# Kernel optimization log

Hardware: AMD Instinct MI355X
Metric: run time of the kernel (lower is better)

## Reference

```python
import jax, jax.numpy as jnp
import numpy as np

ALPHA = 0.2  # LeakyReLU negative slope


def setup_inputs() -> dict:
    key = jax.random.key(0)
    k1, k2, k3, k4 = jax.random.split(key, 4)
    B, N, Fin, Fout = 8, 2048, 256, 256
    h = jax.random.normal(k1, (B, N, Fin), dtype=jnp.float32)
    # random 0/1 adjacency with guaranteed self-loops so every row has a neighbor
    adj = jax.random.randint(k2, (N, N), 0, 2).astype(jnp.float32)
    adj = jnp.maximum(adj, jnp.eye(N, dtype=jnp.float32))
    # xavier_uniform with gain=1.414
    def xavier(k, shape, gain=1.414):
        fan_in, fan_out = shape[0], shape[1]
        a = gain * np.sqrt(6.0 / (fan_in + fan_out))
        return jax.random.uniform(k, shape, dtype=jnp.float32, minval=-a, maxval=a)
    W = xavier(k3, (Fin, Fout))
    a = xavier(k4, (2 * Fout, 1))
    return {"h": h, "adj_matrix": adj, "W": W, "a": a}


def reference(h, adj_matrix, W, a):
    # h: [B, N, Fin], adj_matrix: [N, N], W: [Fin, Fout], a: [2*Fout, 1]
    Fout = W.shape[1]
    Wh = jnp.einsum("bnf,fo->bno", h, W)            # [B, N, Fout]
    a1, a2 = a[:Fout, 0], a[Fout:, 0]                 # split additive attention vector
    # e[b,i,j] = leakyrelu(Wh[b,i]@a1 + Wh[b,j]@a2) — equals concat([Wh_i,Wh_j])@a
    s1 = Wh @ a1                                      # [B, N]
    s2 = Wh @ a2                                      # [B, N]
    e = s1[:, :, None] + s2[:, None, :]               # [B, N, N]
    e = jnp.where(e >= 0, e, ALPHA * e)               # LeakyReLU
    e = jnp.where(adj_matrix[None] == 0, -jnp.inf, e)  # mask non-edges
    attention = jax.nn.softmax(e, axis=-1)            # [B, N, N]
    # dropout is identity in eval mode (training=False)
    h_prime = jnp.einsum("bij,bjo->bio", attention, Wh)
    return h_prime
```

## Files before the change

### kernel.cpp

```cpp
#include <hip/hip_runtime.h>
#include <cstdint>

#define NN 2048
#define LOG2E 1.4426950408889634f

typedef __attribute__((ext_vector_type(8))) short bf16x8;
typedef __attribute__((ext_vector_type(4))) float f32x4;

__device__ __forceinline__ unsigned short f2bf(float x){
  union { float f; unsigned u; } v; v.f = x;
  unsigned r = v.u + 0x7FFFu + ((v.u >> 16) & 1u);
  return (unsigned short)(r >> 16);
}
__device__ __forceinline__ unsigned pack2(float a, float b){
  return (unsigned)f2bf(a) | ((unsigned)f2bf(b) << 16);
}
__device__ __forceinline__ unsigned permpack(unsigned hi, unsigned lo){
  return __builtin_amdgcn_perm(hi, lo, 0x07060302u);
}

__global__ __launch_bounds__(256) void k_prep(const float* __restrict__ adj,
                                              const float* __restrict__ W,
                                              unsigned long long* __restrict__ ab,
                                              unsigned short* __restrict__ Wt){
  int tid = threadIdx.x;
  if (blockIdx.x < 2048){
    int i = blockIdx.x;
    int w = tid >> 6, lane = tid & 63;
    #pragma unroll
    for (int seg = 0; seg < 8; seg++){
      int j = seg * 256 + tid;
      unsigned long long m = __ballot(adj[(size_t)i * NN + j] != 0.0f);
      if (lane == 0) ab[i * 32 + seg * 4 + w] = m;
    }
  } else {
    int g = (blockIdx.x - 2048) * 256 + tid;
    int o = g >> 8, k = g & 255;
    Wt[g] = f2bf(W[k * 256 + o]);
  }
}

__global__ __launch_bounds__(512, 2) void k_fused_gemm(const float* __restrict__ h,
                                                       const unsigned short* __restrict__ Wt,
                                                       const float* __restrict__ a,
                                                       unsigned short* __restrict__ WhT,
                                                       float* __restrict__ s1c,
                                                       float* __restrict__ s2c){
  __shared__ __align__(16) unsigned short As[2][64 * 72];
  __shared__ __align__(16) unsigned short Ts[256 * 72];
  __shared__ float s1p[8][64], s2p[8][64];
  const int tid = threadIdx.x;
  const int r0 = blockIdx.x * 64;
  const int b  = r0 >> 11;
  const int i0 = r0 & (NN - 1);
  const int w = tid >> 6, lane = tid & 63, lhi = lane >> 4, llo = lane & 15;
  const int wc = w * 32;

  f32x4 acc[4][2];
  #pragma unroll
  for (int i = 0; i < 4; i++)
    #pragma unroll
    for (int j = 0; j < 2; j++){ acc[i][j][0]=0.f; acc[i][j][1]=0.f; acc[i][j][2]=0.f; acc[i][j][3]=0.f; }

  const int ar = tid >> 3;
  const int as_ = (tid & 7) * 8;

  float4 hv[4][2];
  #pragma unroll
  for (int t = 0; t < 4; t++){
    const float* hp = h + (size_t)(r0 + ar) * 256 + t * 64 + as_;
    hv[t][0] = *(const float4*)hp;
    hv[t][1] = *(const float4*)(hp + 4);
  }

  auto loadB = [&](int k0, bf16x8* dst){
    #pragma unroll
    for (int ot = 0; ot < 2; ot++)
      #pragma unroll
      for (int kk = 0; kk < 2; kk++)
        dst[ot * 2 + kk] = *(const bf16x8*)(Wt + (size_t)(wc + ot * 16 + llo) * 256 + k0 + kk * 32 + lhi * 8);
  };

  bf16x8 bfr[2][4];
  loadB(0, bfr[0]);

  #pragma unroll
  for (int t = 0; t < 4; t++){
    uint4 q = make_uint4(pack2(hv[t][0].x, hv[t][0].y), pack2(hv[t][0].z, hv[t][0].w),
                         pack2(hv[t][1].x, hv[t][1].y), pack2(hv[t][1].z, hv[t][1].w));
    *(uint4*)&As[t & 1][ar * 72 + as_] = q;
    __syncthreads();
    if (t < 3) loadB((t + 1) * 64, bfr[(t + 1) & 1]);
    bf16x8 af[2][4];
    #pragma unroll
    for (int kk = 0; kk < 2; kk++)
      #pragma unroll
      for (int it = 0; it < 4; it++)
        af[kk][it] = *(const bf16x8*)&As[t & 1][(it * 16 + llo) * 72 + kk * 32 + lhi * 8];
    #pragma unroll
    for (int kk = 0; kk < 2; kk++)
      #pragma unroll
      for (int it = 0; it < 4; it++)
        #pragma unroll
        for (int ot = 0; ot < 2; ot++)
          acc[it][ot] = __builtin_amdgcn_mfma_f32_16x16x32_bf16(af[kk][it], bfr[t & 1][ot * 2 + kk], acc[it][ot], 0, 0, 0);
  }

  float a1v[2], a2v[2];
  #pragma unroll
  for (int ot = 0; ot < 2; ot++){
    a1v[ot] = a[wc + ot * 16 + llo] * LOG2E;
    a2v[ot] = a[256 + wc + ot * 16 + llo] * LOG2E;
  }
  #pragma unroll
  for (int it = 0; it < 4; it++){
    #pragma unroll
    for (int q = 0; q < 4; q++){
      float p1 = acc[it][0][q] * a1v[0] + acc[it][1][q] * a1v[1];
      float p2 = acc[it][0][q] * a2v[0] + acc[it][1][q] * a2v[1];
      #pragma unroll
      for (int o = 1; o < 16; o <<= 1){ p1 += __shfl_xor(p1, o); p2 += __shfl_xor(p2, o); }
      if (llo == 0){
        s1p[w][it * 16 + lhi * 4 + q] = p1;
        s2p[w][it * 16 + lhi * 4 + q] = p2;
      }
    }
  }

  #pragma unroll
  for (int it = 0; it < 4; it++){
    #pragma unroll
    for (int ot = 0; ot < 2; ot++){
      int o = wc + ot * 16 + llo;
      uint2 u = make_uint2(pack2(acc[it][ot][0], acc[it][ot][1]),
                           pack2(acc[it][ot][2], acc[it][ot][3]));
      *(uint2*)&Ts[o * 72 + it * 16 + lhi * 4] = u;
    }
  }
  __syncthreads();

  if (tid < 64){
    float t1 = 0.f, t2 = 0.f;
    #pragma unroll
    for (int g = 0; g < 8; g++){ t1 += s1p[g][tid]; t2 += s2p[g][tid]; }
    s1c[r0 + tid] = t1;
    s2c[r0 + tid] = t2;
  }
  #pragma unroll
  for (int p = 0; p < 4; p++){
    int o = p * 64 + (tid >> 3), col = (tid & 7) * 8;
    *(uint4*)(WhT + (size_t)(b * 256 + o) * 2048 + i0 + col) = *(const uint4*)&Ts[o * 72 + col];
  }
}

__global__ __launch_bounds__(512, 2) void k_attn(const float* __restrict__ s1c,
                                                 const float* __restrict__ s2c,
                                                 const unsigned short* __restrict__ WhT,
                                                 const unsigned long long* __restrict__ ab,
                                                 float* __restrict__ out){
  __shared__ __align__(16) float s2s[2048];
  __shared__ __align__(16) unsigned short Ps[2][64 * 72];
  __shared__ __align__(16) unsigned char bitsB[64 * 264];
  __shared__ float s1s[64], lin[64], red[8];
  const int tid = threadIdx.x;
  const int bid = blockIdx.x;
  const int b = bid & 7, i0 = (bid >> 3) * 64;
  const int w = tid >> 6, lane = tid & 63, lhi = lane >> 4, llo = lane & 15;
  const int wc = w * 32;

  float4 v = ((const float4*)(s2c + (size_t)b * NN))[tid];
  ((float4*)s2s)[tid] = v;
  float vmax = fmaxf(fmaxf(v.x, v.y), fmaxf(v.z, v.w));
  #pragma unroll
  for (int o = 32; o; o >>= 1) vmax = fmaxf(vmax, __shfl_xor(vmax, o));
  if (lane == 0) red[w] = vmax;
  if (tid < 64) s1s[tid] = s1c[(size_t)b * NN + i0 + tid];
  #pragma unroll
  for (int k = 0; k < 4; k++){
    int g = k * 512 + tid;
    unsigned long long mw = ab[(size_t)i0 * 32 + g];
    *(unsigned long long*)&bitsB[(g >> 5) * 264 + (g & 31) * 8] = mw;
  }
  __syncthreads();
  float m2 = red[0];
  #pragma unroll
  for (int g = 1; g < 8; g++) m2 = fmaxf(m2, red[g]);

  const int pi = tid >> 3;
  const int e8 = tid & 7;
  const int pj = e8 * 8;
  const float s1v = s1s[pi];
  const float xm = s1v + m2;
  const float mv = fmaxf(xm, 0.2f * xm);
  const float c1 = s1v - mv;
  const float c2 = 0.2f * s1v - mv;
  float rs = 0.f;

  f32x4 acc[4][2];
  #pragma unroll
  for (int i = 0; i < 4; i++)
    #pragma unroll
    for (int j = 0; j < 2; j++){ acc[i][j][0]=0.f; acc[i][j][1]=0.f; acc[i][j][2]=0.f; acc[i][j][3]=0.f; }

  auto loadB = [&](int j0, bf16x8* dst){
    #pragma unroll
    for (int ot = 0; ot < 2; ot++)
      #pragma unroll
      for (int kk = 0; kk < 2; kk++)
        dst[ot * 2 + kk] = *(const bf16x8*)(WhT + (size_t)(b * 256 + wc + ot * 16 + llo) * 2048 + j0 + kk * 32 + lhi * 8);
  };

  unsigned pu[8];
  auto computeP = [&](int tn){
    unsigned bits = bitsB[pi * 264 + tn * 8 + e8];
    const float* sp = &s2s[tn * 64 + pj];
    float4 xa = *(const float4*)sp;
    float4 xb = *(const float4*)(sp + 4);
    float xs[8] = {xa.x, xa.y, xa.z, xa.w, xb.x, xb.y, xb.z, xb.w};
    #pragma unroll
    for (int e = 0; e < 8; e++){
      float s2v = xs[e];
      float y = fmaxf(s2v + c1, __builtin_fmaf(0.2f, s2v, c2));
      float p = __builtin_amdgcn_exp2f(y);
      unsigned m = ((bits >> e) & 1u) ? 0xFFFF0000u : 0u;
      unsigned u = __float_as_uint(p) & m;
      rs += __uint_as_float(u);
      pu[e] = u;
    }
  };

  auto stageBody = [&](int t, int BUF, bf16x8* curB, bf16x8* nxtB, bool last){
    uint4 q = make_uint4(permpack(pu[1], pu[0]), permpack(pu[3], pu[2]),
                         permpack(pu[5], pu[4]), permpack(pu[7], pu[6]));
    *(uint4*)&Ps[BUF][pi * 72 + pj] = q;
    __syncthreads();
    if (!last) loadB((t + 1) * 64, nxtB);
    bf16x8 af[2][4];
    #pragma unroll
    for (int kk = 0; kk < 2; kk++)
      #pragma unroll
      for (int it = 0; it < 4; it++)
        af[kk][it] = *(const bf16x8*)&Ps[BUF][(it * 16 + llo) * 72 + kk * 32 + lhi * 8];
    if (!last) computeP(t + 1);
    #pragma unroll
    for (int kk = 0; kk < 2; kk++)
      #pragma unroll
      for (int it = 0; it < 4; it++)
        #pragma unroll
        for (int ot = 0; ot < 2; ot++)
          acc[it][ot] = __builtin_amdgcn_mfma_f32_16x16x32_bf16(af[kk][it], curB[ot * 2 + kk], acc[it][ot], 0, 0, 0);
  };

  bf16x8 bA[4], bB[4];
  loadB(0, bA);
  computeP(0);
  for (int t2 = 0; t2 < 32; t2 += 2){
    stageBody(t2,     0, bA, bB, false);
    stageBody(t2 + 1, 1, bB, bA, t2 + 1 == 31);
  }

  rs += __shfl_xor(rs, 1);
  rs += __shfl_xor(rs, 2);
  rs += __shfl_xor(rs, 4);
  if (e8 == 0) lin[pi] = 1.0f / rs;
  __syncthreads();

  #pragma unroll
  for (int it = 0; it < 4; it++){
    #pragma unroll
    for (int ot = 0; ot < 2; ot++){
      int col = wc + ot * 16 + llo;
      #pragma unroll
      for (int q = 0; q < 4; q++){
        int row = it * 16 + lhi * 4 + q;
        out[(size_t)(b * NN + i0 + row) * 256 + col] = acc[it][ot][q] * lin[row];
      }
    }
  }
}

extern "C" void kernel_launch(void* const* d_in, const int* in_sizes, int n_in,
                              void* d_out, int out_size, void* d_ws, size_t ws_size,
                              hipStream_t stream) {
  const float* h   = (const float*)d_in[0];
  const float* adj = (const float*)d_in[1];
  const float* W   = (const float*)d_in[2];
  const float* a   = (const float*)d_in[3];
  float* out = (float*)d_out;

  char* ws = (char*)d_ws;
  unsigned short* WhT      = (unsigned short*)(ws);
  unsigned short* Wt       = (unsigned short*)(ws + 8388608);
  unsigned long long* ab   = (unsigned long long*)(ws + 8519680);
  float* s1c               = (float*)(ws + 9043968);
  float* s2c               = (float*)(ws + 9109504);

  hipLaunchKernelGGL(k_prep,       dim3(2304), dim3(256), 0, stream, adj, W, ab, Wt);
  hipLaunchKernelGGL(k_fused_gemm, dim3(256),  dim3(512), 0, stream, h, Wt, a, WhT, s1c, s2c);
  hipLaunchKernelGGL(k_attn,       dim3(256),  dim3(512), 0, stream, s1c, s2c, WhT, ab, out);
}
```

Measured before the change: 136.6 us.

## Shrink row tiles and split attention output columns across more blocks

Both kernels move from 512-thread blocks with 64-row tiles to 256-thread blocks with 32-row tiles. The projection GEMM grid grows to 512 blocks, and the attention kernel grid grows to 1024 blocks by also splitting the 256 output columns into two halves of 128. The aim is more resident waves per CU to hide latency, and to fill the GPU better than one large block per CU. The cost is that each attention row's softmax probabilities (exp and mask work) are now computed twice, once per column half. The WhT tile is fetched per half, and the s2 vector and mask bits are loaded per block. A sync is also added before overwriting the double-buffered A tile in the GEMM.

```diff
diff --git a/kernel.cpp b/kernel.cpp
--- a/kernel.cpp
+++ b/kernel.cpp
@@ -40,27 +40,27 @@
   }
 }
 
-__global__ __launch_bounds__(512, 2) void k_fused_gemm(const float* __restrict__ h,
+__global__ __launch_bounds__(256, 2) void k_fused_gemm(const float* __restrict__ h,
                                                        const unsigned short* __restrict__ Wt,
                                                        const float* __restrict__ a,
                                                        unsigned short* __restrict__ WhT,
                                                        float* __restrict__ s1c,
                                                        float* __restrict__ s2c){
-  __shared__ __align__(16) unsigned short As[2][64 * 72];
-  __shared__ __align__(16) unsigned short Ts[256 * 72];
-  __shared__ float s1p[8][64], s2p[8][64];
+  __shared__ __align__(16) unsigned short As[2][32 * 72];
+  __shared__ __align__(16) unsigned short Ts[256 * 40];
+  __shared__ float s1p[4][32], s2p[4][32];
   const int tid = threadIdx.x;
-  const int r0 = blockIdx.x * 64;
+  const int r0 = blockIdx.x * 32;
   const int b  = r0 >> 11;
   const int i0 = r0 & (NN - 1);
   const int w = tid >> 6, lane = tid & 63, lhi = lane >> 4, llo = lane & 15;
-  const int wc = w * 32;
-
-  f32x4 acc[4][2];
-  #pragma unroll
-  for (int i = 0; i < 4; i++)
-    #pragma unroll
-    for (int j = 0; j < 2; j++){ acc[i][j][0]=0.f; acc[i][j][1]=0.f; acc[i][j][2]=0.f; acc[i][j][3]=0.f; }
+  const int wc = w * 64;
+
+  f32x4 acc[2][4];
+  #pragma unroll
+  for (int i = 0; i < 2; i++)
+    #pragma unroll
+    for (int j = 0; j < 4; j++){ acc[i][j][0]=0.f; acc[i][j][1]=0.f; acc[i][j][2]=0.f; acc[i][j][3]=0.f; }
 
   const int ar = tid >> 3;
   const int as_ = (tid & 7) * 8;
@@ -75,49 +75,54 @@
 
   auto loadB = [&](int k0, bf16x8* dst){
     #pragma unroll
-    for (int ot = 0; ot < 2; ot++)
+    for (int ot = 0; ot < 4; ot++)
       #pragma unroll
       for (int kk = 0; kk < 2; kk++)
         dst[ot * 2 + kk] = *(const bf16x8*)(Wt + (size_t)(wc + ot * 16 + llo) * 256 + k0 + kk * 32 + lhi * 8);
   };
 
-  bf16x8 bfr[2][4];
+  bf16x8 bfr[2][8];
   loadB(0, bfr[0]);
 
   #pragma unroll
   for (int t = 0; t < 4; t++){
     uint4 q = make_uint4(pack2(hv[t][0].x, hv[t][0].y), pack2(hv[t][0].z, hv[t][0].w),
                          pack2(hv[t][1].x, hv[t][1].y), pack2(hv[t][1].z, hv[t][1].w));
+    if (t) __syncthreads();
     *(uint4*)&As[t & 1][ar * 72 + as_] = q;
     __syncthreads();
     if (t < 3) loadB((t + 1) * 64, bfr[(t + 1) & 1]);
-    bf16x8 af[2][4];
+    bf16x8 af[2][2];
     #pragma unroll
     for (int kk = 0; kk < 2; kk++)
       #pragma unroll
-      for (int it = 0; it < 4; it++)
+      for (int it = 0; it < 2; it++)
         af[kk][it] = *(const bf16x8*)&As[t & 1][(it * 16 + llo) * 72 + kk * 32 + lhi * 8];
     #pragma unroll
     for (int kk = 0; kk < 2; kk++)
       #pragma unroll
-      for (int it = 0; it < 4; it++)
+      for (int it = 0; it < 2; it++)
         #pragma unroll
-        for (int ot = 0; ot < 2; ot++)
+        for (int ot = 0; ot < 4; ot++)
           acc[it][ot] = __builtin_amdgcn_mfma_f32_16x16x32_bf16(af[kk][it], bfr[t & 1][ot * 2 + kk], acc[it][ot], 0, 0, 0);
   }
 
-  float a1v[2], a2v[2];
-  #pragma unroll
-  for (int ot = 0; ot < 2; ot++){
+  float a1v[4], a2v[4];
+  #pragma unroll
+  for (int ot = 0; ot < 4; ot++){
     a1v[ot] = a[wc + ot * 16 + llo] * LOG2E;
     a2v[ot] = a[256 + wc + ot * 16 + llo] * LOG2E;
   }
   #pragma unroll
-  for (int it = 0; it < 4; it++){
+  for (int it = 0; it < 2; it++){
     #pragma unroll
     for (int q = 0; q < 4; q++){
-      float p1 = acc[it][0][q] * a1v[0] + acc[it][1][q] * a1v[1];
-      float p2 = acc[it][0][q] * a2v[0] + acc[it][1][q] * a2v[1];
+      float p1 = 0.f, p2 = 0.f;
+      #pragma unroll
+      for (int ot = 0; ot < 4; ot++){
+        p1 += acc[it][ot][q] * a1v[ot];
+        p2 += acc[it][ot][q] * a2v[ot];
+      }
       #pragma unroll
       for (int o = 1; o < 16; o <<= 1){ p1 += __shfl_xor(p1, o); p2 += __shfl_xor(p2, o); }
       if (llo == 0){
@@ -128,63 +133,67 @@
   }
 
   #pragma unroll
-  for (int it = 0; it < 4; it++){
-    #pragma unroll
-    for (int ot = 0; ot < 2; ot++){
+  for (int it = 0; it < 2; it++){
+    #pragma unroll
+    for (int ot = 0; ot < 4; ot++){
       int o = wc + ot * 16 + llo;
       uint2 u = make_uint2(pack2(acc[it][ot][0], acc[it][ot][1]),
                            pack2(acc[it][ot][2], acc[it][ot][3]));
-      *(uint2*)&Ts[o * 72 + it * 16 + lhi * 4] = u;
+      *(uint2*)&Ts[o * 40 + it * 16 + lhi * 4] = u;
     }
   }
   __syncthreads();
 
-  if (tid < 64){
+  if (tid < 32){
     float t1 = 0.f, t2 = 0.f;
     #pragma unroll
-    for (int g = 0; g < 8; g++){ t1 += s1p[g][tid]; t2 += s2p[g][tid]; }
+    for (int g = 0; g < 4; g++){ t1 += s1p[g][tid]; t2 += s2p[g][tid]; }
     s1c[r0 + tid] = t1;
     s2c[r0 + tid] = t2;
   }
   #pragma unroll
   for (int p = 0; p < 4; p++){
-    int o = p * 64 + (tid >> 3), col = (tid & 7) * 8;
-    *(uint4*)(WhT + (size_t)(b * 256 + o) * 2048 + i0 + col) = *(const uint4*)&Ts[o * 72 + col];
-  }
-}
-
-__global__ __launch_bounds__(512, 2) void k_attn(const float* __restrict__ s1c,
+    int o = p * 64 + (tid >> 2), col = (tid & 3) * 8;
+    *(uint4*)(WhT + (size_t)(b * 256 + o) * 2048 + i0 + col) = *(const uint4*)&Ts[o * 40 + col];
+  }
+}
+
+__global__ __launch_bounds__(256, 4) void k_attn(const float* __restrict__ s1c,
                                                  const float* __restrict__ s2c,
                                                  const unsigned short* __restrict__ WhT,
                                                  const unsigned long long* __restrict__ ab,
                                                  float* __restrict__ out){
   __shared__ __align__(16) float s2s[2048];
-  __shared__ __align__(16) unsigned short Ps[2][64 * 72];
-  __shared__ __align__(16) unsigned char bitsB[64 * 264];
-  __shared__ float s1s[64], lin[64], red[8];
+  __shared__ __align__(16) unsigned short Ps[2][32 * 72];
+  __shared__ __align__(16) unsigned char bitsB[32 * 264];
+  __shared__ float s1s[32], lin[32], red[4];
   const int tid = threadIdx.x;
   const int bid = blockIdx.x;
-  const int b = bid & 7, i0 = (bid >> 3) * 64;
+  const int b = bid & 7;
+  const int r = bid >> 3;
+  const int i0 = (r & 63) * 32;
+  const int o0 = (r >> 6) * 128;
   const int w = tid >> 6, lane = tid & 63, lhi = lane >> 4, llo = lane & 15;
-  const int wc = w * 32;
-
-  float4 v = ((const float4*)(s2c + (size_t)b * NN))[tid];
-  ((float4*)s2s)[tid] = v;
-  float vmax = fmaxf(fmaxf(v.x, v.y), fmaxf(v.z, v.w));
+  const int co = o0 + w * 32;
+
+  float4 v0 = ((const float4*)(s2c + (size_t)b * NN))[tid];
+  float4 v1 = ((const float4*)(s2c + (size_t)b * NN))[tid + 256];
+  ((float4*)s2s)[tid]       = v0;
+  ((float4*)s2s)[tid + 256] = v1;
+  float vmax = fmaxf(fmaxf(fmaxf(v0.x, v0.y), fmaxf(v0.z, v0.w)),
+                     fmaxf(fmaxf(v1.x, v1.y), fmaxf(v1.z, v1.w)));
   #pragma unroll
   for (int o = 32; o; o >>= 1) vmax = fmaxf(vmax, __shfl_xor(vmax, o));
   if (lane == 0) red[w] = vmax;
-  if (tid < 64) s1s[tid] = s1c[(size_t)b * NN + i0 + tid];
+  if (tid < 32) s1s[tid] = s1c[(size_t)b * NN + i0 + tid];
   #pragma unroll
   for (int k = 0; k < 4; k++){
-    int g = k * 512 + tid;
+    int g = k * 256 + tid;
     unsigned long long mw = ab[(size_t)i0 * 32 + g];
     *(unsigned long long*)&bitsB[(g >> 5) * 264 + (g & 31) * 8] = mw;
   }
   __syncthreads();
-  float m2 = red[0];
-  #pragma unroll
-  for (int g = 1; g < 8; g++) m2 = fmaxf(m2, red[g]);
+  float m2 = fmaxf(fmaxf(red[0], red[1]), fmaxf(red[2], red[3]));
 
   const int pi = tid >> 3;
   const int e8 = tid & 7;
@@ -196,9 +205,9 @@
   const float c2 = 0.2f * s1v - mv;
   float rs = 0.f;
 
-  f32x4 acc[4][2];
-  #pragma unroll
-  for (int i = 0; i < 4; i++)
+  f32x4 acc[2][2];
+  #pragma unroll
+  for (int i = 0; i < 2; i++)
     #pragma unroll
     for (int j = 0; j < 2; j++){ acc[i][j][0]=0.f; acc[i][j][1]=0.f; acc[i][j][2]=0.f; acc[i][j][3]=0.f; }
 
@@ -207,7 +216,7 @@
     for (int ot = 0; ot < 2; ot++)
       #pragma unroll
       for (int kk = 0; kk < 2; kk++)
-        dst[ot * 2 + kk] = *(const bf16x8*)(WhT + (size_t)(b * 256 + wc + ot * 16 + llo) * 2048 + j0 + kk * 32 + lhi * 8);
+        dst[ot * 2 + kk] = *(const bf16x8*)(WhT + (size_t)(b * 256 + co + ot * 16 + llo) * 2048 + j0 + kk * 32 + lhi * 8);
   };
 
   unsigned pu[8];
@@ -235,17 +244,17 @@
     *(uint4*)&Ps[BUF][pi * 72 + pj] = q;
     __syncthreads();
     if (!last) loadB((t + 1) * 64, nxtB);
-    bf16x8 af[2][4];
+    bf16x8 af[2][2];
     #pragma unroll
     for (int kk = 0; kk < 2; kk++)
       #pragma unroll
-      for (int it = 0; it < 4; it++)
+      for (int it = 0; it < 2; it++)
         af[kk][it] = *(const bf16x8*)&Ps[BUF][(it * 16 + llo) * 72 + kk * 32 + lhi * 8];
     if (!last) computeP(t + 1);
     #pragma unroll
     for (int kk = 0; kk < 2; kk++)
       #pragma unroll
-      for (int it = 0; it < 4; it++)
+      for (int it = 0; it < 2; it++)
         #pragma unroll
         for (int ot = 0; ot < 2; ot++)
           acc[it][ot] = __builtin_amdgcn_mfma_f32_16x16x32_bf16(af[kk][it], curB[ot * 2 + kk], acc[it][ot], 0, 0, 0);
@@ -266,10 +275,10 @@
   __syncthreads();
 
   #pragma unroll
-  for (int it = 0; it < 4; it++){
+  for (int it = 0; it < 2; it++){
     #pragma unroll
     for (int ot = 0; ot < 2; ot++){
-      int col = wc + ot * 16 + llo;
+      int col = co + ot * 16 + llo;
       #pragma unroll
       for (int q = 0; q < 4; q++){
         int row = it * 16 + lhi * 4 + q;
@@ -296,6 +305,6 @@
   float* s2c               = (float*)(ws + 9109504);
 
   hipLaunchKernelGGL(k_prep,       dim3(2304), dim3(256), 0, stream, adj, W, ab, Wt);
-  hipLaunchKernelGGL(k_fused_gemm, dim3(256),  dim3(512), 0, stream, h, Wt, a, WhT, s1c, s2c);
-  hipLaunchKernelGGL(k_attn,       dim3(256),  dim3(512), 0, stream, s1c, s2c, WhT, ab, out);
-}
+  hipLaunchKernelGGL(k_fused_gemm, dim3(512),  dim3(256), 0, stream, h, Wt, a, WhT, s1c, s2c);
+  hipLaunchKernelGGL(k_attn,       dim3(1024), dim3(256), 0, stream, s1c, s2c, WhT, ab, out);
+}
```

After: 157.1 us. +15.0%, slower.

## Store A/P tiles in MFMA-fragment order for contiguous conflict-free LDS access

Applied to the files above, without the earlier changes.

Both kernels now have each thread produce exactly the bf16x8 fragment that an MFMA lane later reads, with wave w owning fragment (it=w>>1, kk=w&1). The shared tiles are stored as contiguous 16-byte-per-lane blocks instead of padded row-major, so writes and fragment reads are linear and free of bank conflicts. In the attention kernel this changes which rows and columns each thread computes P for, so the row-sum reduction now uses lane shuffles plus a cross-wave shared-memory pass and one extra barrier.

```diff
diff --git a/kernel.cpp b/kernel.cpp
--- a/kernel.cpp
+++ b/kernel.cpp
@@ -46,7 +46,7 @@
                                                        unsigned short* __restrict__ WhT,
                                                        float* __restrict__ s1c,
                                                        float* __restrict__ s2c){
-  __shared__ __align__(16) unsigned short As[2][64 * 72];
+  __shared__ __align__(16) unsigned char As[2 * 8192];
   __shared__ __align__(16) unsigned short Ts[256 * 72];
   __shared__ float s1p[8][64], s2p[8][64];
   const int tid = threadIdx.x;
@@ -55,6 +55,9 @@
   const int i0 = r0 & (NN - 1);
   const int w = tid >> 6, lane = tid & 63, lhi = lane >> 4, llo = lane & 15;
   const int wc = w * 32;
+  const int sit = w >> 1, skk = w & 1;
+  const int srow = sit * 16 + llo;
+  const int skol = skk * 32 + lhi * 8;
 
   f32x4 acc[4][2];
   #pragma unroll
@@ -62,13 +65,10 @@
     #pragma unroll
     for (int j = 0; j < 2; j++){ acc[i][j][0]=0.f; acc[i][j][1]=0.f; acc[i][j][2]=0.f; acc[i][j][3]=0.f; }
 
-  const int ar = tid >> 3;
-  const int as_ = (tid & 7) * 8;
-
   float4 hv[4][2];
   #pragma unroll
   for (int t = 0; t < 4; t++){
-    const float* hp = h + (size_t)(r0 + ar) * 256 + t * 64 + as_;
+    const float* hp = h + (size_t)(r0 + srow) * 256 + t * 64 + skol;
     hv[t][0] = *(const float4*)hp;
     hv[t][1] = *(const float4*)(hp + 4);
   }
@@ -80,7 +80,6 @@
       for (int kk = 0; kk < 2; kk++)
         dst[ot * 2 + kk] = *(const bf16x8*)(Wt + (size_t)(wc + ot * 16 + llo) * 256 + k0 + kk * 32 + lhi * 8);
   };
-
   bf16x8 bfr[2][4];
   loadB(0, bfr[0]);
 
@@ -88,7 +87,7 @@
   for (int t = 0; t < 4; t++){
     uint4 q = make_uint4(pack2(hv[t][0].x, hv[t][0].y), pack2(hv[t][0].z, hv[t][0].w),
                          pack2(hv[t][1].x, hv[t][1].y), pack2(hv[t][1].z, hv[t][1].w));
-    *(uint4*)&As[t & 1][ar * 72 + as_] = q;
+    *(uint4*)&As[(t & 1) * 8192 + w * 1024 + lane * 16] = q;
     __syncthreads();
     if (t < 3) loadB((t + 1) * 64, bfr[(t + 1) & 1]);
     bf16x8 af[2][4];
@@ -96,7 +95,7 @@
     for (int kk = 0; kk < 2; kk++)
       #pragma unroll
       for (int it = 0; it < 4; it++)
-        af[kk][it] = *(const bf16x8*)&As[t & 1][(it * 16 + llo) * 72 + kk * 32 + lhi * 8];
+        af[kk][it] = *(const bf16x8*)&As[(t & 1) * 8192 + (it * 2 + kk) * 1024 + lane * 16];
     #pragma unroll
     for (int kk = 0; kk < 2; kk++)
       #pragma unroll
@@ -159,14 +158,16 @@
                                                  const unsigned long long* __restrict__ ab,
                                                  float* __restrict__ out){
   __shared__ __align__(16) float s2s[2048];
-  __shared__ __align__(16) unsigned short Ps[2][64 * 72];
+  __shared__ __align__(16) unsigned char PsB[2 * 8192];
   __shared__ __align__(16) unsigned char bitsB[64 * 264];
-  __shared__ float s1s[64], lin[64], red[8];
+  __shared__ float s1s[64], lin[64], red[8], rsp[8][64];
   const int tid = threadIdx.x;
   const int bid = blockIdx.x;
   const int b = bid & 7, i0 = (bid >> 3) * 64;
   const int w = tid >> 6, lane = tid & 63, lhi = lane >> 4, llo = lane & 15;
   const int wc = w * 32;
+  const int sit = w >> 1, skk = w & 1;
+  const int prow = sit * 16 + llo;
 
   float4 v = ((const float4*)(s2c + (size_t)b * NN))[tid];
   ((float4*)s2s)[tid] = v;
@@ -186,10 +187,7 @@
   #pragma unroll
   for (int g = 1; g < 8; g++) m2 = fmaxf(m2, red[g]);
 
-  const int pi = tid >> 3;
-  const int e8 = tid & 7;
-  const int pj = e8 * 8;
-  const float s1v = s1s[pi];
+  const float s1v = s1s[prow];
   const float xm = s1v + m2;
   const float mv = fmaxf(xm, 0.2f * xm);
   const float c1 = s1v - mv;
@@ -210,13 +208,14 @@
         dst[ot * 2 + kk] = *(const bf16x8*)(WhT + (size_t)(b * 256 + wc + ot * 16 + llo) * 2048 + j0 + kk * 32 + lhi * 8);
   };
 
-  unsigned pu[8];
+  unsigned puq[4];
   auto computeP = [&](int tn){
-    unsigned bits = bitsB[pi * 264 + tn * 8 + e8];
-    const float* sp = &s2s[tn * 64 + pj];
+    unsigned bits = bitsB[prow * 264 + tn * 8 + skk * 4 + lhi];
+    const float* sp = &s2s[tn * 64 + skk * 32 + lhi * 8];
     float4 xa = *(const float4*)sp;
     float4 xb = *(const float4*)(sp + 4);
     float xs[8] = {xa.x, xa.y, xa.z, xa.w, xb.x, xb.y, xb.z, xb.w};
+    unsigned pu[8];
     #pragma unroll
     for (int e = 0; e < 8; e++){
       float s2v = xs[e];
@@ -227,12 +226,12 @@
       rs += __uint_as_float(u);
       pu[e] = u;
     }
+    puq[0] = permpack(pu[1], pu[0]); puq[1] = permpack(pu[3], pu[2]);
+    puq[2] = permpack(pu[5], pu[4]); puq[3] = permpack(pu[7], pu[6]);
   };
 
   auto stageBody = [&](int t, int BUF, bf16x8* curB, bf16x8* nxtB, bool last){
-    uint4 q = make_uint4(permpack(pu[1], pu[0]), permpack(pu[3], pu[2]),
-                         permpack(pu[5], pu[4]), permpack(pu[7], pu[6]));
-    *(uint4*)&Ps[BUF][pi * 72 + pj] = q;
+    *(uint4*)&PsB[BUF * 8192 + w * 1024 + lane * 16] = *(uint4*)&puq[0];
     __syncthreads();
     if (!last) loadB((t + 1) * 64, nxtB);
     bf16x8 af[2][4];
@@ -240,7 +239,7 @@
     for (int kk = 0; kk < 2; kk++)
       #pragma unroll
       for (int it = 0; it < 4; it++)
-        af[kk][it] = *(const bf16x8*)&Ps[BUF][(it * 16 + llo) * 72 + kk * 32 + lhi * 8];
+        af[kk][it] = *(const bf16x8*)&PsB[BUF * 8192 + (it * 2 + kk) * 1024 + lane * 16];
     if (!last) computeP(t + 1);
     #pragma unroll
     for (int kk = 0; kk < 2; kk++)
@@ -259,10 +258,14 @@
     stageBody(t2 + 1, 1, bB, bA, t2 + 1 == 31);
   }
 
-  rs += __shfl_xor(rs, 1);
-  rs += __shfl_xor(rs, 2);
-  rs += __shfl_xor(rs, 4);
-  if (e8 == 0) lin[pi] = 1.0f / rs;
+  rs += __shfl_xor(rs, 16);
+  rs += __shfl_xor(rs, 32);
+  if (lhi == 0) rsp[w][prow] = rs;
+  __syncthreads();
+  if (tid < 64){
+    int it = tid >> 4;
+    lin[tid] = 1.0f / (rsp[it * 2][tid] + rsp[it * 2 + 1][tid]);
+  }
   __syncthreads();
 
   #pragma unroll
```

Result: no change. 134.4 us (-1.6%).
